# Kernel tuning notes

Hardware: AMD Instinct MI355X
Metric: run time of the kernel (lower is better)

## Reference

```python
import jax, jax.numpy as jnp
import numpy as np

N_NODES = 100000
N_EDGES = 3200000
IN_F, HID, OUT_F = 256, 128, 8


def gcn_conv(x, src, dst, W, b, n_nodes):
    # PyG GCNConv: linear transform, add self-loops, symmetric normalization, scatter-add, bias
    x = x @ W  # [N, F_out]
    loop = jnp.arange(n_nodes, dtype=src.dtype)
    src_f = jnp.concatenate([src, loop])
    dst_f = jnp.concatenate([dst, loop])
    ones = jnp.ones(src_f.shape[0], dtype=x.dtype)
    deg = jax.ops.segment_sum(ones, dst_f, num_segments=n_nodes)  # in-degree incl self-loop
    dinv = jax.lax.rsqrt(jnp.maximum(deg, 1e-12))
    norm = dinv[src_f] * dinv[dst_f]  # [E+N]
    msgs = x[src_f] * norm[:, None]
    out = jax.ops.segment_sum(msgs, dst_f, num_segments=n_nodes)
    return out + b


def setup_inputs() -> dict:
    key = jax.random.key(0)
    k1, k2, k3, k4 = jax.random.split(key, 4)
    x = jax.random.normal(k1, (N_NODES, IN_F), dtype=jnp.float32)
    edge_index = jax.random.randint(k2, (2, N_EDGES), 0, N_NODES, dtype=jnp.int64)
    W1 = jax.random.normal(k3, (IN_F, HID), dtype=jnp.float32) * (1.0 / np.sqrt(IN_F))
    b1 = jnp.zeros((HID,), dtype=jnp.float32)
    W2 = jax.random.normal(k4, (HID, OUT_F), dtype=jnp.float32) * (1.0 / np.sqrt(HID))
    b2 = jnp.zeros((OUT_F,), dtype=jnp.float32)
    return {"x": x, "edge_index": edge_index, "W1": W1, "b1": b1, "W2": W2, "b2": b2}


def reference(x, edge_index, W1, b1, W2, b2):
    n_nodes = x.shape[0]
    src, dst = edge_index[0], edge_index[1]
    h = gcn_conv(x, src, dst, W1, b1, n_nodes)
    h = jax.nn.relu(h)
    h = gcn_conv(h, src, dst, W2, b2, n_nodes)
    return jax.nn.log_softmax(h, axis=1)
```

## Files before the change

### kernel.cpp

```cpp
#include <hip/hip_runtime.h>
#include <hip/hip_bf16.h>
#include <stdint.h>

#define N_NODES 100000
#define N_EDGES 3200000
#define IN_F 256
#define HID 128
#define OUT_F 8

#define NB   391
#define PASS 6144
#define CAP  10240

typedef short short8 __attribute__((ext_vector_type(8)));
typedef float f32x4 __attribute__((ext_vector_type(4)));
typedef float f32x2 __attribute__((ext_vector_type(2)));


__device__ __forceinline__ uint32_t pk_bf16(float a, float b) {
    uint32_t ua = __float_as_uint(a);
    uint32_t ub = __float_as_uint(b);
    ua = (ua + 0x7fff + ((ua >> 16) & 1)) >> 16;
    ub = (ub + 0x7fff + ((ub >> 16) & 1)) & 0xffff0000u;
    return ua | ub;
}

__global__ __launch_bounds__(256) void k_bhist(const int* __restrict__ dst,
                                               int* __restrict__ gcnt, int E) {
    __shared__ int lb[NB];
    for (int i = threadIdx.x; i < NB; i += 256) lb[i] = 0;
    __syncthreads();
    int stride = gridDim.x * 256;
    const int4* d4 = (const int4*)dst;
    for (int e = blockIdx.x * 256 + threadIdx.x; e < E / 4; e += stride) {
        int4 d = d4[e];
        atomicAdd(&lb[d.x >> 8], 1);
        atomicAdd(&lb[d.y >> 8], 1);
        atomicAdd(&lb[d.z >> 8], 1);
        atomicAdd(&lb[d.w >> 8], 1);
    }
    __syncthreads();
    for (int i = threadIdx.x; i < NB; i += 256) {
        int c = lb[i];
        if (c) atomicAdd(&gcnt[i * 64], c);
    }
}

__global__ __launch_bounds__(512) void k_bscan(const int* __restrict__ gcnt,
                                               int* __restrict__ bbase,
                                               int* __restrict__ gcur) {
    __shared__ int sc[512];
    int tid = threadIdx.x;
    int v = (tid < NB) ? gcnt[tid * 64] : 0;
    sc[tid] = v;
    __syncthreads();
    for (int d = 1; d < 512; d <<= 1) {
        int t = (tid >= d) ? sc[tid - d] : 0;
        __syncthreads();
        sc[tid] += t;
        __syncthreads();
    }
    int excl = sc[tid] - v;
    if (tid <= NB) bbase[tid] = excl;
    if (tid < NB) gcur[tid * 64] = excl;
}

__global__ __launch_bounds__(512) void k_part(const int* __restrict__ src,
                                              const int* __restrict__ dst,
                                              int* __restrict__ gcur,
                                              uint32_t* __restrict__ epk, int E) {
    __shared__ int lcnt[NB], loff[NB], ladj[NB], lcur[NB];
    __shared__ int sc[512];
    __shared__ uint32_t stage[PASS];
    int tid = threadIdx.x;
    int e0 = blockIdx.x * PASS;

    for (int i = tid; i < NB; i += 512) { lcnt[i] = 0; lcur[i] = 0; }
    __syncthreads();
    for (int i = tid; i < PASS; i += 512) {
        int e = e0 + i;
        if (e < E) atomicAdd(&lcnt[dst[e] >> 8], 1);
    }
    __syncthreads();
    int v = (tid < NB) ? lcnt[tid] : 0;
    sc[tid] = v;
    __syncthreads();
    for (int d = 1; d < 512; d <<= 1) {
        int t = (tid >= d) ? sc[tid - d] : 0;
        __syncthreads();
        sc[tid] += t;
        __syncthreads();
    }
    if (tid < NB) loff[tid] = sc[tid] - v;
    __syncthreads();
    if (tid < NB) {
        int len = lcnt[tid];
        if (len > 0) ladj[tid] = atomicAdd(&gcur[tid * 64], len);
    }
    __syncthreads();
    for (int i = tid; i < PASS; i += 512) {
        int e = e0 + i;
        if (e < E) {
            int d = dst[e];
            int b = d >> 8;
            int r = atomicAdd(&lcur[b], 1);
            stage[loff[b] + r] = (uint32_t)src[e] | ((uint32_t)(d & 255) << 17);
        }
    }
    __syncthreads();
    int wv = tid >> 6, ln = tid & 63;
    int sub = ln >> 4, l16 = ln & 15;
    for (int b = wv * 4 + sub; b < NB; b += 32) {
        int len = lcnt[b];
        if (len) {
            int lo = loff[b], gb = ladj[b];
            for (int j = l16; j < len; j += 16) epk[gb + j] = stage[lo + j];
        }
    }
}

__global__ __launch_bounds__(1024) void k_csr(const uint32_t* __restrict__ epk,
                                              const int* __restrict__ bbase,
                                              int* __restrict__ offs,
                                              int* __restrict__ cnt,
                                              float* __restrict__ dinv,
                                              int* __restrict__ ssrc, int N) {
    __shared__ int lcnt[256], lcur[256], loff[256];
    __shared__ uint32_t stage[CAP];
    int tid = threadIdx.x, b = blockIdx.x;
    int base = bbase[b], m = bbase[b + 1] - base;

    if (tid < 256) lcnt[tid] = 0;
    __syncthreads();
    for (int i = tid; i < m; i += 1024)
        atomicAdd(&lcnt[(epk[base + i] >> 17) & 255], 1);
    __syncthreads();
    int v = (tid < 256) ? lcnt[tid] : 0;
    if (tid < 256) loff[tid] = v;
    __syncthreads();
    for (int d = 1; d < 256; d <<= 1) {
        int t = (tid >= d && tid < 256) ? loff[tid - d] : 0;
        __syncthreads();
        if (tid < 256) loff[tid] += t;
        __syncthreads();
    }
    int excl = (tid < 256) ? (loff[tid] - v) : 0;
    __syncthreads();
    if (tid < 256) {
        loff[tid] = excl;
        lcur[tid] = 0;
        int node = b * 256 + tid;
        if (node < N) {
            offs[node] = base + excl;
            cnt[node] = v;
            dinv[node] = rsqrtf((float)(v + 1));
        }
    }
    __syncthreads();
    if (m <= CAP) {
        for (int i = tid; i < m; i += 1024) {
            uint32_t u = epk[base + i];
            int ld = (u >> 17) & 255;
            int r = atomicAdd(&lcur[ld], 1);
            stage[loff[ld] + r] = u & 0x1FFFF;
        }
        __syncthreads();
        for (int i = tid; i < m; i += 1024) ssrc[base + i] = (int)stage[i];
    } else {
        for (int i = tid; i < m; i += 1024) {
            uint32_t u = epk[base + i];
            int ld = (u >> 17) & 255;
            int r = atomicAdd(&lcur[ld], 1);
            ssrc[base + loff[ld] + r] = (int)(u & 0x1FFFF);
        }
    }
}

__global__ __launch_bounds__(256) void k_wcast(const float* __restrict__ W1,
                                               ushort* __restrict__ Wbf) {
    __shared__ ushort T[128][33];
    int t = threadIdx.x;
    int k0 = blockIdx.x * 32;
    for (int idx = t; idx < 32 * 128; idx += 256) {
        int k = idx >> 7, n = idx & 127;
        uint32_t uv = __float_as_uint(W1[(size_t)(k0 + k) * HID + n]);
        uv = (uv + 0x7fff + ((uv >> 16) & 1)) >> 16;
        T[n][k] = (ushort)uv;
    }
    __syncthreads();
    for (int idx = t; idx < 32 * 128; idx += 256) {
        int n = idx >> 5, k = idx & 31;
        Wbf[(size_t)n * IN_F + k0 + k] = T[n][k];
    }
}

__global__ __launch_bounds__(256) void k_gemm1(const float* __restrict__ X,
                                               const ushort* __restrict__ Wbf,
                                               const float* __restrict__ dinv,
                                               uint32_t* __restrict__ Hs8, int M) {
    __shared__ uint32_t As[64 * 20];
    __shared__ uint32_t Bs[128 * 20];
    int t = threadIdx.x;
    int lane = t & 63, w = t >> 6;
    int q = lane >> 4, c16 = lane & 15;
    int row0 = blockIdx.x * 64;

    int ar = t >> 2, a4 = (t & 3);
    int grow = row0 + ar; if (grow >= M) grow = M - 1;
    const float* xrow = X + (size_t)grow * IN_F;
    int bn = t >> 1, b1h = (t & 1);
    const ushort* wrow = Wbf + (size_t)bn * IN_F;

    f32x4 acc[8];
    #pragma unroll
    for (int j = 0; j < 8; j++) acc[j] = (f32x4){0.f, 0.f, 0.f, 0.f};

    for (int kc = 0; kc < IN_F; kc += 32) {
        float4 x0 = *(const float4*)(xrow + kc + a4 * 8);
        float4 x1 = *(const float4*)(xrow + kc + a4 * 8 + 4);
        uint4 wv0 = *(const uint4*)(wrow + kc + b1h * 16);
        uint4 wv1 = *(const uint4*)(wrow + kc + b1h * 16 + 8);
        __syncthreads();
        *(uint2*)&As[ar * 20 + a4 * 4]     = make_uint2(pk_bf16(x0.x, x0.y), pk_bf16(x0.z, x0.w));
        *(uint2*)&As[ar * 20 + a4 * 4 + 2] = make_uint2(pk_bf16(x1.x, x1.y), pk_bf16(x1.z, x1.w));
        *(uint4*)&Bs[bn * 20 + b1h * 8]     = wv0;
        *(uint4*)&Bs[bn * 20 + b1h * 8 + 4] = wv1;
        __syncthreads();
        short8 af = *(const short8*)&As[(w * 16 + c16) * 20 + q * 4];
        #pragma unroll
        for (int j = 0; j < 8; j++) {
            short8 bf = *(const short8*)&Bs[(j * 16 + c16) * 20 + q * 4];
            acc[j] = __builtin_amdgcn_mfma_f32_16x16x32_bf16(af, bf, acc[j], 0, 0, 0);
        }
    }
    float dv[4];
    #pragma unroll
    for (int r = 0; r < 4; r++) {
        int gr = row0 + w * 16 + q * 4 + r;
        dv[r] = (gr < M) ? dinv[gr] : 0.f;
    }
    #pragma unroll
    for (int r = 0; r < 4; r++) {
        int gr = row0 + w * 16 + q * 4 + r;
        uint32_t lo = 0, hi = 0;
        lo = __builtin_amdgcn_cvt_pk_fp8_f32(acc[0][r] * dv[r], acc[1][r] * dv[r], lo, false);
        lo = __builtin_amdgcn_cvt_pk_fp8_f32(acc[2][r] * dv[r], acc[3][r] * dv[r], lo, true);
        hi = __builtin_amdgcn_cvt_pk_fp8_f32(acc[4][r] * dv[r], acc[5][r] * dv[r], hi, false);
        hi = __builtin_amdgcn_cvt_pk_fp8_f32(acc[6][r] * dv[r], acc[7][r] * dv[r], hi, true);
        if (gr < M) *(uint2*)&Hs8[(size_t)gr * 32 + c16 * 2] = make_uint2(lo, hi);
    }
}

__global__ __launch_bounds__(256) void k_agg1(const uint32_t* __restrict__ hs,
                                              const int* __restrict__ offs,
                                              const int* __restrict__ cnt,
                                              const float* __restrict__ dinv,
                                              const int* __restrict__ ssrc,
                                              const float* __restrict__ b1,
                                              const float* __restrict__ W2,
                                              uint32_t* __restrict__ h2bf, int N) {
    __shared__ float w2t[OUT_F * HID];
    __shared__ float b1p[HID];
    int t = threadIdx.x;
    for (int i = t; i < OUT_F * HID; i += 256) {
        int f = i >> 7, rem = i & 127;
        int cc = rem >> 2, bb = rem & 3;
        int feat = ((cc & 1) * 4 + bb) * 16 + (cc >> 1);
        w2t[i] = W2[feat * OUT_F + f];
    }
    if (t < HID) {
        int cc = t >> 2, bb = t & 3;
        b1p[t] = b1[((cc & 1) * 4 + bb) * 16 + (cc >> 1)];
    }
    __syncthreads();
    int wid = (blockIdx.x * 256 + t) >> 6;
    int lane = t & 63;
    if (wid >= N) return;
    int h = lane >> 5, c = lane & 31;
    float dv = dinv[wid];
    f32x2 s01 = {0.f, 0.f}, s23 = {0.f, 0.f};
    if (h == 0) {
        uint32_t u = hs[(size_t)wid * 32 + c];
        s01 = __builtin_amdgcn_cvt_pk_f32_fp8(u, false);
        s23 = __builtin_amdgcn_cvt_pk_f32_fp8(u, true);
    }
    int beg = offs[wid], n = cnt[wid];
    const int* sp = ssrc + beg;
    int j = h;
    for (; j + 14 < n; j += 16) {
        int e0 = sp[j],      e1 = sp[j + 2],  e2 = sp[j + 4],  e3 = sp[j + 6];
        int e4 = sp[j + 8],  e5 = sp[j + 10], e6 = sp[j + 12], e7 = sp[j + 14];
        uint32_t u0 = hs[(size_t)e0 * 32 + c];
        uint32_t u1 = hs[(size_t)e1 * 32 + c];
        uint32_t u2 = hs[(size_t)e2 * 32 + c];
        uint32_t u3 = hs[(size_t)e3 * 32 + c];
        uint32_t u4 = hs[(size_t)e4 * 32 + c];
        uint32_t u5 = hs[(size_t)e5 * 32 + c];
        uint32_t u6 = hs[(size_t)e6 * 32 + c];
        uint32_t u7 = hs[(size_t)e7 * 32 + c];
        s01 += __builtin_amdgcn_cvt_pk_f32_fp8(u0, false); s23 += __builtin_amdgcn_cvt_pk_f32_fp8(u0, true);
        s01 += __builtin_amdgcn_cvt_pk_f32_fp8(u1, false); s23 += __builtin_amdgcn_cvt_pk_f32_fp8(u1, true);
        s01 += __builtin_amdgcn_cvt_pk_f32_fp8(u2, false); s23 += __builtin_amdgcn_cvt_pk_f32_fp8(u2, true);
        s01 += __builtin_amdgcn_cvt_pk_f32_fp8(u3, false); s23 += __builtin_amdgcn_cvt_pk_f32_fp8(u3, true);
        s01 += __builtin_amdgcn_cvt_pk_f32_fp8(u4, false); s23 += __builtin_amdgcn_cvt_pk_f32_fp8(u4, true);
        s01 += __builtin_amdgcn_cvt_pk_f32_fp8(u5, false); s23 += __builtin_amdgcn_cvt_pk_f32_fp8(u5, true);
        s01 += __builtin_amdgcn_cvt_pk_f32_fp8(u6, false); s23 += __builtin_amdgcn_cvt_pk_f32_fp8(u6, true);
        s01 += __builtin_amdgcn_cvt_pk_f32_fp8(u7, false); s23 += __builtin_amdgcn_cvt_pk_f32_fp8(u7, true);
    }
    for (; j + 6 < n; j += 8) {
        int e0 = sp[j], e1 = sp[j + 2], e2 = sp[j + 4], e3 = sp[j + 6];
        uint32_t u0 = hs[(size_t)e0 * 32 + c];
        uint32_t u1 = hs[(size_t)e1 * 32 + c];
        uint32_t u2 = hs[(size_t)e2 * 32 + c];
        uint32_t u3 = hs[(size_t)e3 * 32 + c];
        s01 += __builtin_amdgcn_cvt_pk_f32_fp8(u0, false); s23 += __builtin_amdgcn_cvt_pk_f32_fp8(u0, true);
        s01 += __builtin_amdgcn_cvt_pk_f32_fp8(u1, false); s23 += __builtin_amdgcn_cvt_pk_f32_fp8(u1, true);
        s01 += __builtin_amdgcn_cvt_pk_f32_fp8(u2, false); s23 += __builtin_amdgcn_cvt_pk_f32_fp8(u2, true);
        s01 += __builtin_amdgcn_cvt_pk_f32_fp8(u3, false); s23 += __builtin_amdgcn_cvt_pk_f32_fp8(u3, true);
    }
    for (; j < n; j += 2) {
        uint32_t u = hs[(size_t)sp[j] * 32 + c];
        s01 += __builtin_amdgcn_cvt_pk_f32_fp8(u, false);
        s23 += __builtin_amdgcn_cvt_pk_f32_fp8(u, true);
    }
    s01[0] += __shfl_xor(s01[0], 32);
    s01[1] += __shfl_xor(s01[1], 32);
    s23[0] += __shfl_xor(s23[0], 32);
    s23[1] += __shfl_xor(s23[1], 32);
    float4 bb = *(const float4*)(b1p + c * 4);
    float o0 = fmaxf(fmaf(s01[0], dv, bb.x), 0.f);
    float o1 = fmaxf(fmaf(s01[1], dv, bb.y), 0.f);
    float o2 = fmaxf(fmaf(s23[0], dv, bb.z), 0.f);
    float o3 = fmaxf(fmaf(s23[1], dv, bb.w), 0.f);
    int f0 = h * 4;
    float p[4];
    #pragma unroll
    for (int f = 0; f < 4; f++) {
        float4 wv = *(const float4*)&w2t[(f0 + f) * HID + c * 4];
        p[f] = o0 * wv.x + o1 * wv.y + o2 * wv.z + o3 * wv.w;
    }
    #pragma unroll
    for (int d = 1; d < 32; d <<= 1) {
        #pragma unroll
        for (int f = 0; f < 4; f++) p[f] += __shfl_xor(p[f], d);
    }
    if (c == 0) {
        uint32_t w0 = pk_bf16(p[0] * dv, p[1] * dv);
        uint32_t w1 = pk_bf16(p[2] * dv, p[3] * dv);
        *(uint2*)&h2bf[(size_t)wid * 4 + h * 2] = make_uint2(w0, w1);
    }
}

__global__ __launch_bounds__(256) void k_agg2(const uint32_t* __restrict__ h2bf,
                                              const int* __restrict__ offs,
                                              const int* __restrict__ cnt,
                                              const float* __restrict__ dinv,
                                              const int* __restrict__ ssrc,
                                              const float* __restrict__ b2,
                                              float* __restrict__ out, int N) {
    int wid = (blockIdx.x * 256 + threadIdx.x) >> 6;
    int lane = threadIdx.x & 63;
    if (wid >= N) return;
    int f2 = lane & 3, g = lane >> 2;
    float dv = dinv[wid];
    int beg = offs[wid], n = cnt[wid];
    const int* sp = ssrc + beg;
    float a0 = 0.f, a1 = 0.f;
    int j = g;
    for (; j + 48 < n; j += 64) {
        int s0 = sp[j], s1 = sp[j + 16], s2 = sp[j + 32], s3 = sp[j + 48];
        uint32_t v0 = h2bf[(size_t)s0 * 4 + f2];
        uint32_t v1 = h2bf[(size_t)s1 * 4 + f2];
        uint32_t v2 = h2bf[(size_t)s2 * 4 + f2];
        uint32_t v3 = h2bf[(size_t)s3 * 4 + f2];
        a0 += __uint_as_float(v0 << 16) + __uint_as_float(v1 << 16)
            + __uint_as_float(v2 << 16) + __uint_as_float(v3 << 16);
        a1 += __uint_as_float(v0 & 0xffff0000u) + __uint_as_float(v1 & 0xffff0000u)
            + __uint_as_float(v2 & 0xffff0000u) + __uint_as_float(v3 & 0xffff0000u);
    }
    for (; j < n; j += 16) {
        uint32_t v = h2bf[(size_t)sp[j] * 4 + f2];
        a0 += __uint_as_float(v << 16);
        a1 += __uint_as_float(v & 0xffff0000u);
    }
    a0 += __shfl_xor(a0, 4);  a1 += __shfl_xor(a1, 4);
    a0 += __shfl_xor(a0, 8);  a1 += __shfl_xor(a1, 8);
    a0 += __shfl_xor(a0, 16); a1 += __shfl_xor(a1, 16);
    a0 += __shfl_xor(a0, 32); a1 += __shfl_xor(a1, 32);
    uint32_t vs = h2bf[(size_t)wid * 4 + f2];
    a0 += __uint_as_float(vs << 16);
    a1 += __uint_as_float(vs & 0xffff0000u);
    float acc0 = fmaf(a0, dv, b2[f2 * 2]);
    float acc1 = fmaf(a1, dv, b2[f2 * 2 + 1]);
    float m = fmaxf(acc0, acc1);
    m = fmaxf(m, __shfl_xor(m, 1));
    m = fmaxf(m, __shfl_xor(m, 2));
    float e = expf(acc0 - m) + expf(acc1 - m);
    e += __shfl_xor(e, 1);
    e += __shfl_xor(e, 2);
    float ls = logf(e);
    if (g == 0) {
        float2 r = make_float2(acc0 - m - ls, acc1 - m - ls);
        *(float2*)&out[(size_t)wid * OUT_F + f2 * 2] = r;
    }
}

extern "C" void kernel_launch(void* const* d_in, const int* in_sizes, int n_in,
                              void* d_out, int out_size, void* d_ws, size_t ws_size,
                              hipStream_t stream) {
    const float* x   = (const float*)d_in[0];
    const int*   ei  = (const int*)d_in[1];
    const float* W1  = (const float*)d_in[2];
    const float* b1  = (const float*)d_in[3];
    const float* W2  = (const float*)d_in[4];
    const float* b2  = (const float*)d_in[5];
    float* out = (float*)d_out;

    const int N = N_NODES, E = N_EDGES;
    const int* src = ei;
    const int* dst = ei + E;

    char* p = (char*)d_ws;
    auto carve = [&](size_t bytes) -> void* {
        void* r = (void*)p;
        p += (bytes + 511) & ~(size_t)511;
        return r;
    };
    int*      gcnt  = (int*)carve((size_t)NB * 64 * 4);
    int*      gcur  = (int*)carve((size_t)NB * 64 * 4);
    int*      bbase = (int*)carve((size_t)(NB + 1) * 4);
    uint32_t* epk   = (uint32_t*)carve((size_t)E * 4);
    int*      offs  = (int*)carve((size_t)N * 4);
    int*      cnt   = (int*)carve((size_t)N * 4);
    float*    dinv  = (float*)carve((size_t)N * 4);
    int*      ssrc  = (int*)carve((size_t)E * 4);
    ushort*   wbf   = (ushort*)carve((size_t)HID * IN_F * 2);
    uint32_t* hs8   = (uint32_t*)carve((size_t)N * 32 * 4);
    uint32_t* h2bf  = (uint32_t*)carve((size_t)N * 4 * 4);

    hipMemsetAsync(gcnt, 0, (size_t)NB * 64 * 4, stream);

    k_wcast<<<8, 256, 0, stream>>>(W1, wbf);
    k_bhist<<<512, 256, 0, stream>>>(dst, gcnt, E);
    k_bscan<<<1, 512, 0, stream>>>(gcnt, bbase, gcur);
    k_part<<<(E + PASS - 1) / PASS, 512, 0, stream>>>(src, dst, gcur, epk, E);
    k_csr<<<NB, 1024, 0, stream>>>(epk, bbase, offs, cnt, dinv, ssrc, N);

    k_gemm1<<<(N + 63) / 64, 256, 0, stream>>>(x, wbf, dinv, hs8, N);
    k_agg1<<<(N * 64 + 255) / 256, 256, 0, stream>>>(hs8, offs, cnt, dinv, ssrc, b1, W2, h2bf, N);
    k_agg2<<<(N * 64 + 255) / 256, 256, 0, stream>>>(h2bf, offs, cnt, dinv, ssrc, b2, out, N);
}
```

Baseline: 376.2 us.

## Replace two-level bucketed CSR build with global atomic degree count and scatter

Swaps the bucket histogram, partition and per-bucket local sort for a simpler CSR build: per-node global atomic degree counting, a three-kernel prefix scan, and a scatter that places each edge's source using global atomic cursors. The aim is to drop the intermediate packed-edge pass and its shared-memory staging. In exchange it relies on many contended global atomics and fully random scattered writes. The order of neighbours within each node becomes nondeterministic, which only changes the order of floating-point summation.

```diff
diff --git a/kernel.cpp b/kernel.cpp
--- a/kernel.cpp
+++ b/kernel.cpp
@@ -8,9 +8,7 @@
 #define HID 128
 #define OUT_F 8
 
-#define NB   391
-#define PASS 6144
-#define CAP  10240
+#define NBLK 391
 
 typedef short short8 __attribute__((ext_vector_type(8)));
 typedef float f32x4 __attribute__((ext_vector_type(4)));
@@ -25,33 +23,43 @@
     return ua | ub;
 }
 
-__global__ __launch_bounds__(256) void k_bhist(const int* __restrict__ dst,
-                                               int* __restrict__ gcnt, int E) {
-    __shared__ int lb[NB];
-    for (int i = threadIdx.x; i < NB; i += 256) lb[i] = 0;
+__global__ __launch_bounds__(256) void k_deg(const int* __restrict__ dst,
+                                             int* __restrict__ cnt, int E4) {
+    const int4* d4 = (const int4*)dst;
+    int stride = gridDim.x * 256;
+    for (int e = blockIdx.x * 256 + threadIdx.x; e < E4; e += stride) {
+        int4 d = d4[e];
+        atomicAdd(&cnt[d.x], 1);
+        atomicAdd(&cnt[d.y], 1);
+        atomicAdd(&cnt[d.z], 1);
+        atomicAdd(&cnt[d.w], 1);
+    }
+}
+
+__global__ __launch_bounds__(256) void k_scan1(const int* __restrict__ cnt,
+                                               int* __restrict__ offs,
+                                               int* __restrict__ bsum, int N) {
+    __shared__ int sc[256];
+    int tid = threadIdx.x;
+    int node = blockIdx.x * 256 + tid;
+    int v = (node < N) ? cnt[node] : 0;
+    sc[tid] = v;
     __syncthreads();
-    int stride = gridDim.x * 256;
-    const int4* d4 = (const int4*)dst;
-    for (int e = blockIdx.x * 256 + threadIdx.x; e < E / 4; e += stride) {
-        int4 d = d4[e];
-        atomicAdd(&lb[d.x >> 8], 1);
-        atomicAdd(&lb[d.y >> 8], 1);
-        atomicAdd(&lb[d.z >> 8], 1);
-        atomicAdd(&lb[d.w >> 8], 1);
-    }
-    __syncthreads();
-    for (int i = threadIdx.x; i < NB; i += 256) {
-        int c = lb[i];
-        if (c) atomicAdd(&gcnt[i * 64], c);
-    }
-}
-
-__global__ __launch_bounds__(512) void k_bscan(const int* __restrict__ gcnt,
-                                               int* __restrict__ bbase,
-                                               int* __restrict__ gcur) {
+    for (int d = 1; d < 256; d <<= 1) {
+        int t = (tid >= d) ? sc[tid - d] : 0;
+        __syncthreads();
+        sc[tid] += t;
+        __syncthreads();
+    }
+    if (node < N) offs[node] = sc[tid] - v;
+    if (tid == 255) bsum[blockIdx.x] = sc[255];
+}
+
+__global__ __launch_bounds__(512) void k_scan2(const int* __restrict__ bsum,
+                                               int* __restrict__ bbase) {
     __shared__ int sc[512];
     int tid = threadIdx.x;
-    int v = (tid < NB) ? gcnt[tid * 64] : 0;
+    int v = (tid < NBLK) ? bsum[tid] : 0;
     sc[tid] = v;
     __syncthreads();
     for (int d = 1; d < 512; d <<= 1) {
@@ -60,119 +68,41 @@
         sc[tid] += t;
         __syncthreads();
     }
-    int excl = sc[tid] - v;
-    if (tid <= NB) bbase[tid] = excl;
-    if (tid < NB) gcur[tid * 64] = excl;
-}
-
-__global__ __launch_bounds__(512) void k_part(const int* __restrict__ src,
-                                              const int* __restrict__ dst,
-                                              int* __restrict__ gcur,
-                                              uint32_t* __restrict__ epk, int E) {
-    __shared__ int lcnt[NB], loff[NB], ladj[NB], lcur[NB];
-    __shared__ int sc[512];
-    __shared__ uint32_t stage[PASS];
-    int tid = threadIdx.x;
-    int e0 = blockIdx.x * PASS;
-
-    for (int i = tid; i < NB; i += 512) { lcnt[i] = 0; lcur[i] = 0; }
-    __syncthreads();
-    for (int i = tid; i < PASS; i += 512) {
-        int e = e0 + i;
-        if (e < E) atomicAdd(&lcnt[dst[e] >> 8], 1);
-    }
-    __syncthreads();
-    int v = (tid < NB) ? lcnt[tid] : 0;
-    sc[tid] = v;
-    __syncthreads();
-    for (int d = 1; d < 512; d <<= 1) {
-        int t = (tid >= d) ? sc[tid - d] : 0;
-        __syncthreads();
-        sc[tid] += t;
-        __syncthreads();
-    }
-    if (tid < NB) loff[tid] = sc[tid] - v;
-    __syncthreads();
-    if (tid < NB) {
-        int len = lcnt[tid];
-        if (len > 0) ladj[tid] = atomicAdd(&gcur[tid * 64], len);
-    }
-    __syncthreads();
-    for (int i = tid; i < PASS; i += 512) {
-        int e = e0 + i;
-        if (e < E) {
-            int d = dst[e];
-            int b = d >> 8;
-            int r = atomicAdd(&lcur[b], 1);
-            stage[loff[b] + r] = (uint32_t)src[e] | ((uint32_t)(d & 255) << 17);
-        }
-    }
-    __syncthreads();
-    int wv = tid >> 6, ln = tid & 63;
-    int sub = ln >> 4, l16 = ln & 15;
-    for (int b = wv * 4 + sub; b < NB; b += 32) {
-        int len = lcnt[b];
-        if (len) {
-            int lo = loff[b], gb = ladj[b];
-            for (int j = l16; j < len; j += 16) epk[gb + j] = stage[lo + j];
-        }
-    }
-}
-
-__global__ __launch_bounds__(1024) void k_csr(const uint32_t* __restrict__ epk,
-                                              const int* __restrict__ bbase,
-                                              int* __restrict__ offs,
-                                              int* __restrict__ cnt,
-                                              float* __restrict__ dinv,
-                                              int* __restrict__ ssrc, int N) {
-    __shared__ int lcnt[256], lcur[256], loff[256];
-    __shared__ uint32_t stage[CAP];
-    int tid = threadIdx.x, b = blockIdx.x;
-    int base = bbase[b], m = bbase[b + 1] - base;
-
-    if (tid < 256) lcnt[tid] = 0;
-    __syncthreads();
-    for (int i = tid; i < m; i += 1024)
-        atomicAdd(&lcnt[(epk[base + i] >> 17) & 255], 1);
-    __syncthreads();
-    int v = (tid < 256) ? lcnt[tid] : 0;
-    if (tid < 256) loff[tid] = v;
-    __syncthreads();
-    for (int d = 1; d < 256; d <<= 1) {
-        int t = (tid >= d && tid < 256) ? loff[tid - d] : 0;
-        __syncthreads();
-        if (tid < 256) loff[tid] += t;
-        __syncthreads();
-    }
-    int excl = (tid < 256) ? (loff[tid] - v) : 0;
-    __syncthreads();
-    if (tid < 256) {
-        loff[tid] = excl;
-        lcur[tid] = 0;
-        int node = b * 256 + tid;
-        if (node < N) {
-            offs[node] = base + excl;
-            cnt[node] = v;
-            dinv[node] = rsqrtf((float)(v + 1));
-        }
-    }
-    __syncthreads();
-    if (m <= CAP) {
-        for (int i = tid; i < m; i += 1024) {
-            uint32_t u = epk[base + i];
-            int ld = (u >> 17) & 255;
-            int r = atomicAdd(&lcur[ld], 1);
-            stage[loff[ld] + r] = u & 0x1FFFF;
-        }
-        __syncthreads();
-        for (int i = tid; i < m; i += 1024) ssrc[base + i] = (int)stage[i];
-    } else {
-        for (int i = tid; i < m; i += 1024) {
-            uint32_t u = epk[base + i];
-            int ld = (u >> 17) & 255;
-            int r = atomicAdd(&lcur[ld], 1);
-            ssrc[base + loff[ld] + r] = (int)(u & 0x1FFFF);
-        }
+    if (tid < NBLK) bbase[tid] = sc[tid] - v;
+}
+
+__global__ __launch_bounds__(256) void k_scan3(const int* __restrict__ cnt,
+                                               const int* __restrict__ bbase,
+                                               int* __restrict__ offs,
+                                               int* __restrict__ cur,
+                                               float* __restrict__ dinv, int N) {
+    int node = blockIdx.x * 256 + threadIdx.x;
+    if (node < N) {
+        int o = offs[node] + bbase[blockIdx.x];
+        offs[node] = o;
+        cur[node] = o;
+        dinv[node] = rsqrtf((float)(cnt[node] + 1));
+    }
+}
+
+__global__ __launch_bounds__(256) void k_scatter(const int* __restrict__ src,
+                                                 const int* __restrict__ dst,
+                                                 int* __restrict__ cur,
+                                                 int* __restrict__ ssrc, int E4) {
+    const int4* s4 = (const int4*)src;
+    const int4* d4 = (const int4*)dst;
+    int stride = gridDim.x * 256;
+    for (int e = blockIdx.x * 256 + threadIdx.x; e < E4; e += stride) {
+        int4 s = s4[e];
+        int4 d = d4[e];
+        int r0 = atomicAdd(&cur[d.x], 1);
+        int r1 = atomicAdd(&cur[d.y], 1);
+        int r2 = atomicAdd(&cur[d.z], 1);
+        int r3 = atomicAdd(&cur[d.w], 1);
+        ssrc[r0] = s.x;
+        ssrc[r1] = s.y;
+        ssrc[r2] = s.z;
+        ssrc[r3] = s.w;
     }
 }
 
@@ -426,25 +356,25 @@
         p += (bytes + 511) & ~(size_t)511;
         return r;
     };
-    int*      gcnt  = (int*)carve((size_t)NB * 64 * 4);
-    int*      gcur  = (int*)carve((size_t)NB * 64 * 4);
-    int*      bbase = (int*)carve((size_t)(NB + 1) * 4);
-    uint32_t* epk   = (uint32_t*)carve((size_t)E * 4);
     int*      offs  = (int*)carve((size_t)N * 4);
     int*      cnt   = (int*)carve((size_t)N * 4);
+    int*      cur   = (int*)carve((size_t)N * 4);
     float*    dinv  = (float*)carve((size_t)N * 4);
+    int*      bsum  = (int*)carve((size_t)NBLK * 4);
+    int*      bbase = (int*)carve((size_t)NBLK * 4);
     int*      ssrc  = (int*)carve((size_t)E * 4);
     ushort*   wbf   = (ushort*)carve((size_t)HID * IN_F * 2);
     uint32_t* hs8   = (uint32_t*)carve((size_t)N * 32 * 4);
     uint32_t* h2bf  = (uint32_t*)carve((size_t)N * 4 * 4);
 
-    hipMemsetAsync(gcnt, 0, (size_t)NB * 64 * 4, stream);
+    hipMemsetAsync(cnt, 0, (size_t)N * 4, stream);
 
     k_wcast<<<8, 256, 0, stream>>>(W1, wbf);
-    k_bhist<<<512, 256, 0, stream>>>(dst, gcnt, E);
-    k_bscan<<<1, 512, 0, stream>>>(gcnt, bbase, gcur);
-    k_part<<<(E + PASS - 1) / PASS, 512, 0, stream>>>(src, dst, gcur, epk, E);
-    k_csr<<<NB, 1024, 0, stream>>>(epk, bbase, offs, cnt, dinv, ssrc, N);
+    k_deg<<<2048, 256, 0, stream>>>(dst, cnt, E / 4);
+    k_scan1<<<NBLK, 256, 0, stream>>>(cnt, offs, bsum, N);
+    k_scan2<<<1, 512, 0, stream>>>(bsum, bbase);
+    k_scan3<<<NBLK, 256, 0, stream>>>(cnt, bbase, offs, cur, dinv, N);
+    k_scatter<<<2048, 256, 0, stream>>>(src, dst, cur, ssrc, E / 4);
 
     k_gemm1<<<(N + 63) / 64, 256, 0, stream>>>(x, wbf, dinv, hs8, N);
     k_agg1<<<(N * 64 + 255) / 256, 256, 0, stream>>>(hs8, offs, cnt, dinv, ssrc, b1, W2, h2bf, N);
```

New measurement: 727.4 us. 93.4% more time.
